# Optimization experiments

Hardware: AMD Instinct MI355X
Metric: run time of the kernel (lower is better)

Reference implementation:

```python
import jax, jax.numpy as jnp
import numpy as np

N, E, G = 50000, 800000, 64
DIMS = [(32, 4, 64), (256, 4, 128), (512, 4, 64)]
EPS = 1e-5  # BatchNorm eps (eval mode, running mean=0, var=1)


def setup_inputs():
    key = jax.random.key(0)
    ks = list(jax.random.split(key, 40))
    it = iter(range(40))
    nxt = lambda: ks[next(it)]
    inp = {}
    inp['x'] = jax.random.normal(nxt(), (N, 32), jnp.float32)
    inp['edge_feature'] = jax.random.normal(nxt(), (E, 6), jnp.float32)
    for li, (fin, H, C) in enumerate(DIMS, 1):
        s = 1.0 / np.sqrt(fin).astype(np.float32)
        inp[f'W{li}'] = jax.random.normal(nxt(), (fin, H * C), jnp.float32) * s
        inp[f'We{li}'] = jax.random.normal(nxt(), (6, H * C), jnp.float32) * 0.3
        inp[f'as{li}'] = jax.random.normal(nxt(), (H, C), jnp.float32) * 0.1
        inp[f'ad{li}'] = jax.random.normal(nxt(), (H, C), jnp.float32) * 0.1
        inp[f'ae{li}'] = jax.random.normal(nxt(), (H, C), jnp.float32) * 0.1
        inp[f'b{li}'] = jnp.zeros((H * C,), jnp.float32)
        inp[f'g{li}'] = jnp.ones((H * C,), jnp.float32)
        inp[f'bb{li}'] = jnp.zeros((H * C,), jnp.float32)
    inp['Wf1'] = jax.random.normal(nxt(), (256, 32), jnp.float32) * 0.0625
    inp['bf1'] = jnp.zeros((32,), jnp.float32)
    inp['gf'] = jnp.ones((32,), jnp.float32)
    inp['bbf'] = jnp.zeros((32,), jnp.float32)
    inp['Wf2'] = jax.random.normal(nxt(), (32, 2), jnp.float32) * 0.2
    inp['bf2'] = jnp.zeros((2,), jnp.float32)
    inp['edge_index'] = jax.random.randint(nxt(), (2, E), 0, N)
    inp['batch'] = jnp.sort(jax.random.randint(nxt(), (N,), 0, G))
    return inp


def _bn(h, g, b):
    # eval-mode BatchNorm1d with running mean 0, running var 1
    return g * h * (1.0 / jnp.sqrt(1.0 + EPS)) + b


def _gat(h, ea, src, dst, W, We, a_s, a_d, a_e, b):
    H, C = a_s.shape
    xs = (h @ W).reshape(N, H, C)                       # shared lin for src/dst
    al_s = jnp.einsum('nhc,hc->nh', xs, a_s)
    al_d = jnp.einsum('nhc,hc->nh', xs, a_d)
    al_e = jnp.einsum('ehc,hc->eh', (ea @ We).reshape(-1, H, C), a_e)
    al = jax.nn.leaky_relu(al_s[src] + al_d[dst] + al_e, 0.2)  # [E+N, H]
    m = jax.ops.segment_max(al, dst, num_segments=N)
    w = jnp.exp(al - m[dst])
    w = w / (jax.ops.segment_sum(w, dst, num_segments=N)[dst] + 1e-16)
    out = jax.ops.segment_sum(xs[src] * w[:, :, None], dst, num_segments=N)
    return out.reshape(N, H * C) + b


def _forward(x, edge_feature, W1, We1, as1, ad1, ae1, b1, g1, bb1,
             W2, We2, as2, ad2, ae2, b2, g2, bb2,
             W3, We3, as3, ad3, ae3, b3, g3, bb3,
             Wf1, bf1, gf, bbf, Wf2, bf2, edge_index, batch):
    src0, dst0 = edge_index[0], edge_index[1]
    # add self loops; self-loop edge_attr = per-dst mean (PyG fill_value='mean')
    deg = jax.ops.segment_sum(jnp.ones((E,), x.dtype), dst0, num_segments=N)
    emean = jax.ops.segment_sum(edge_feature, dst0, num_segments=N) / jnp.maximum(deg, 1.0)[:, None]
    loops = jnp.arange(N)
    src = jnp.concatenate([src0, loops])
    dst = jnp.concatenate([dst0, loops])
    ea = jnp.concatenate([edge_feature, emean], axis=0)
    h = jax.nn.elu(_bn(_gat(x, ea, src, dst, W1, We1, as1, ad1, ae1, b1), g1, bb1))
    h = jax.nn.elu(_bn(_gat(h, ea, src, dst, W2, We2, as2, ad2, ae2, b2), g2, bb2))
    h = jax.nn.elu(_bn(_gat(h, ea, src, dst, W3, We3, as3, ad3, ae3, b3), g3, bb3))
    cnt = jax.ops.segment_sum(jnp.ones((N,), h.dtype), batch, num_segments=G)
    pooled = jax.ops.segment_sum(h, batch, num_segments=G) / jnp.maximum(cnt, 1.0)[:, None]
    h = jax.nn.elu(_bn(pooled @ Wf1 + bf1, gf, bbf))
    return jax.nn.log_softmax(h @ Wf2 + bf2, axis=1)


def reference(x, edge_feature, W1, We1, as1, ad1, ae1, b1, g1, bb1,
              W2, We2, as2, ad2, ae2, b2, g2, bb2,
              W3, We3, as3, ad3, ae3, b3, g3, bb3,
              Wf1, bf1, gf, bbf, Wf2, bf2, edge_index, batch):
    return _forward(x, edge_feature, W1, We1, as1, ad1, ae1, b1, g1, bb1,
                    W2, We2, as2, ad2, ae2, b2, g2, bb2,
                    W3, We3, as3, ad3, ae3, b3, g3, bb3,
                    Wf1, bf1, gf, bbf, Wf2, bf2, edge_index, batch)
```

## Files before the change

### kernel.cpp

```cpp
#include <hip/hip_runtime.h>
#include <cstdint>
#include <cstddef>

#define NN 50000
#define NPAD 50048
#define EE 800000
#define ET (EE + NN)
#define GG 64
#define HH 4
#define RSQ 0.9999950000374997f

typedef short bf16x8 __attribute__((ext_vector_type(8)));
typedef unsigned short u16x8 __attribute__((ext_vector_type(8)));
typedef unsigned short u16x4 __attribute__((ext_vector_type(4)));
typedef float f32x4 __attribute__((ext_vector_type(4)));
typedef float f32x2 __attribute__((ext_vector_type(2)));

__device__ __forceinline__ float bf2f(unsigned short u) {
    union { unsigned int i; float f; } v; v.i = ((unsigned int)u) << 16; return v.f;
}
__device__ __forceinline__ unsigned short f2bf(float f) {
    union { float f; unsigned int i; } v; v.f = f;
    unsigned int u = v.i;
    u += 0x7fffu + ((u >> 16) & 1u);
    return (unsigned short)(u >> 16);
}


#if __has_builtin(__builtin_amdgcn_cvt_pk_fp8_f32) && __has_builtin(__builtin_amdgcn_cvt_pk_f32_fp8)
#define FP8_HW 1
#else
#define FP8_HW 0
#endif

#if !FP8_HW
__device__ __forceinline__ unsigned int enc1_fp8(float f) {
    unsigned int u = __float_as_uint(f);
    unsigned int s = (u >> 24) & 0x80u;
    float a = fabsf(f);
    a = fminf(a, 448.f);
    unsigned int b;
    if (a >= 0.015625f) {
        unsigned int ub = __float_as_uint(a);
        unsigned int mant = ub & 0x7FFFFFu;
        unsigned int keep = mant >> 20;
        unsigned int rem = mant & 0xFFFFFu;
        unsigned int exp = (ub >> 23) - 127u + 7u;
        unsigned int q = (exp << 3) | keep;
        if (rem > 0x80000u || (rem == 0x80000u && (q & 1u))) q++;
        if (q > 0x7Eu) q = 0x7Eu;
        b = q;
    } else {
        int q = (int)(a * 512.0f + 0.5f);
        b = (q > 7) ? 0x08u : (unsigned int)q;
    }
    return s | b;
}
__device__ __forceinline__ float dec1_fp8(unsigned int b) {
    unsigned int sgn = (b & 0x80u) << 24;
    float r;
    if (b & 0x78u) {
        r = __uint_as_float(sgn | (((b & 0x7Fu) + 0x3C0u) << 20));
    } else {
        r = (float)(b & 7u) * 0x1p-9f;
        r = (b & 0x80u) ? -r : r;
    }
    return r;
}
#endif

__device__ __forceinline__ unsigned int pk4_fp8(float f0, float f1, float f2, float f3) {
#if FP8_HW
    int r = __builtin_amdgcn_cvt_pk_fp8_f32(f0, f1, 0, false);
    r = __builtin_amdgcn_cvt_pk_fp8_f32(f2, f3, r, true);
    return (unsigned int)r;
#else
    return enc1_fp8(f0) | (enc1_fp8(f1) << 8) | (enc1_fp8(f2) << 16) | (enc1_fp8(f3) << 24);
#endif
}

__device__ __forceinline__ f32x2 dec2lo_fp8(unsigned int u) {
#if FP8_HW
    return __builtin_amdgcn_cvt_pk_f32_fp8((int)u, false);
#else
    f32x2 r; r[0] = dec1_fp8(u & 0xFFu); r[1] = dec1_fp8((u >> 8) & 0xFFu); return r;
#endif
}
__device__ __forceinline__ f32x2 dec2hi_fp8(unsigned int u) {
#if FP8_HW
    return __builtin_amdgcn_cvt_pk_f32_fp8((int)u, true);
#else
    f32x2 r; r[0] = dec1_fp8((u >> 16) & 0xFFu); r[1] = dec1_fp8(u >> 24); return r;
#endif
}

static inline void* carve(char*& p, size_t bytes) {
    void* r = (void*)p;
    p += (bytes + 255) & ~(size_t)255;
    return r;
}


__global__ void deg_kernel(const int* __restrict__ dst0, int* __restrict__ deg,
                           int* __restrict__ epos) {
    int e = blockIdx.x * blockDim.x + threadIdx.x;
    if (e >= EE) return;
    epos[e] = atomicAdd(&deg[dst0[e]], 1);
}

#define SCAN_B 512
__global__ void scan1_kernel(const int* __restrict__ deg, int* __restrict__ out,
                             int* __restrict__ bsum, int n) {
    __shared__ int tmp[SCAN_B];
    int i = blockIdx.x * SCAN_B + threadIdx.x;
    int v = (i < n) ? (deg[i] + 1) : 0;
    tmp[threadIdx.x] = v;
    __syncthreads();
    for (int off = 1; off < SCAN_B; off <<= 1) {
        int t = (threadIdx.x >= off) ? tmp[threadIdx.x - off] : 0;
        __syncthreads();
        tmp[threadIdx.x] += t;
        __syncthreads();
    }
    if (i < n) out[i] = tmp[threadIdx.x] - v;
    if (threadIdx.x == SCAN_B - 1) bsum[blockIdx.x] = tmp[threadIdx.x];
}

__global__ void scan2_kernel(int* __restrict__ bsum, int nb) {
    __shared__ int tmp[128];
    int v = (threadIdx.x < nb) ? bsum[threadIdx.x] : 0;
    tmp[threadIdx.x] = v;
    __syncthreads();
    for (int off = 1; off < 128; off <<= 1) {
        int t = (threadIdx.x >= off) ? tmp[threadIdx.x - off] : 0;
        __syncthreads();
        tmp[threadIdx.x] += t;
        __syncthreads();
    }
    if (threadIdx.x < nb) bsum[threadIdx.x] = tmp[threadIdx.x] - v;
}

__global__ void scan3_kernel(int* __restrict__ out, const int* __restrict__ bsum, int n) {
    int i = blockIdx.x * SCAN_B + threadIdx.x;
    if (i < n) out[i] += bsum[blockIdx.x];
    if (i == 0 && blockIdx.x == 0) out[n] = ET;
}

__global__ void fill_kernel(const int* __restrict__ src0, const int* __restrict__ dst0,
                            const int* __restrict__ row_ptr, const int* __restrict__ epos,
                            const int* __restrict__ deg,
                            int* __restrict__ ssrc, int* __restrict__ seid) {
    int e = blockIdx.x * blockDim.x + threadIdx.x;
    if (e < EE) {
        int idx = row_ptr[dst0[e]] + epos[e];
        ssrc[idx] = src0[e];
        seid[idx] = e;
    } else if (e < ET) {
        int n = e - EE;
        int idx = row_ptr[n] + deg[n];
        ssrc[idx] = n;
        seid[idx] = EE + n;
    }
}


__global__ void convx_kernel(const float* __restrict__ x, unsigned short* __restrict__ xb) {
    int i = blockIdx.x * blockDim.x + threadIdx.x;
    if (i >= NPAD * 64) return;
    int row = i >> 6, col = i & 63;
    float v = 0.f;
    if (row < NN && col < 32) v = x[(size_t)row * 32 + col];
    xb[i] = f2bf(v);
}

__global__ void convw_all_kernel(const float* __restrict__ W1, const float* __restrict__ W2,
                                 const float* __restrict__ W3,
                                 unsigned short* __restrict__ Wt1,
                                 unsigned short* __restrict__ Wt2,
                                 unsigned short* __restrict__ Wt3) {
    int i = blockIdx.x * blockDim.x + threadIdx.x;
    if (i < 16384) {
        int c = i >> 6, k = i & 63;
        Wt1[i] = (k < 32) ? f2bf(W1[(size_t)k * 256 + c]) : (unsigned short)0;
    } else if (i < 16384 + 131072) {
        int j = i - 16384;
        int c = j >> 8, k = j & 255;
        Wt2[j] = f2bf(W2[(size_t)k * 512 + c]);
    } else if (i < 16384 + 262144) {
        int j = i - 147456;
        int c = j >> 9, k = j & 511;
        Wt3[j] = f2bf(W3[(size_t)k * 256 + c]);
    }
}

__global__ void wea_all_kernel(const float* __restrict__ We1, const float* __restrict__ ae1,
                               const float* __restrict__ We2, const float* __restrict__ ae2,
                               const float* __restrict__ We3, const float* __restrict__ ae3,
                               float* __restrict__ Wea) {
    int t = threadIdx.x;
    if (t >= 72) return;
    int l = t / 24, w = t % 24, k = w / 4, h = w % 4;
    const float* We = (l == 0) ? We1 : (l == 1) ? We2 : We3;
    const float* ae = (l == 0) ? ae1 : (l == 1) ? ae2 : ae3;
    int C = (l == 1) ? 128 : 64;
    int HC = 4 * C;
    float s = 0.f;
    for (int c = 0; c < C; c++) s += We[(size_t)k * HC + h * C + c] * ae[(size_t)h * C + c];
    Wea[l * 24 + k * 4 + h] = s;
}


#if __has_builtin(__builtin_amdgcn_global_load_lds)
#define GLL_OK 1
#else
#define GLL_OK 0
#endif

#define TILE_LD 136

template <int C_>
__global__ __launch_bounds__(256) void gemm_fused_kernel(const unsigned short* __restrict__ A,
                                                         const unsigned short* __restrict__ Bt,
                                                         unsigned char* __restrict__ X8,
                                                         const float* __restrict__ a_s,
                                                         const float* __restrict__ a_d,
                                                         float* __restrict__ als,
                                                         float* __restrict__ ald,
                                                         int K) {
    constexpr int HC = HH * C_;
    __shared__ unsigned short smem[128 * TILE_LD + 64];
    unsigned short* As = smem;
    unsigned short* Bs = smem + 8192;
    const int tid = threadIdx.x;
    const int bm = blockIdx.x * 128;
    const int bn = blockIdx.y * 128;
    const int lane = tid & 63;
    const int wv = tid >> 6;
    const int wrow = (wv >> 1) * 64;
    const int wcol = (wv & 1) * 64;
    const int l15 = lane & 15;
    const int q = lane >> 4;

    f32x4 acc[4][4];
#pragma unroll
    for (int m = 0; m < 4; m++)
#pragma unroll
        for (int n = 0; n < 4; n++) acc[m][n] = (f32x4)0.f;

    for (int k0 = 0; k0 < K; k0 += 64) {
#pragma unroll
        for (int i = 0; i < 4; i++) {
            int c = (wv * 4 + i) * 64 + lane;
            int row = c >> 3, slot = c & 7;
            int slotG = slot ^ (row & 7);
            const unsigned short* ga = &A[(size_t)(bm + row) * K + k0 + slotG * 8];
            const unsigned short* gb = &Bt[(size_t)(bn + row) * K + k0 + slotG * 8];
#if GLL_OK
            __builtin_amdgcn_global_load_lds(
                (const __attribute__((address_space(1))) unsigned int*)ga,
                (__attribute__((address_space(3))) unsigned int*)&As[(size_t)(wv * 4 + i) * 512],
                16, 0, 0);
            __builtin_amdgcn_global_load_lds(
                (const __attribute__((address_space(1))) unsigned int*)gb,
                (__attribute__((address_space(3))) unsigned int*)&Bs[(size_t)(wv * 4 + i) * 512],
                16, 0, 0);
#else
            *(u16x8*)&As[(size_t)c * 8] = *(const u16x8*)ga;
            *(u16x8*)&Bs[(size_t)c * 8] = *(const u16x8*)gb;
#endif
        }
        __syncthreads();
#pragma unroll
        for (int kk = 0; kk < 2; kk++) {
            bf16x8 af[4], bfr[4];
#pragma unroll
            for (int m = 0; m < 4; m++) {
                int ra = wrow + m * 16 + l15;
                af[m] = *(const bf16x8*)&As[ra * 64 + ((kk * 4 + q) ^ (ra & 7)) * 8];
            }
#pragma unroll
            for (int n = 0; n < 4; n++) {
                int rb = wcol + n * 16 + l15;
                bfr[n] = *(const bf16x8*)&Bs[rb * 64 + ((kk * 4 + q) ^ (rb & 7)) * 8];
            }
#pragma unroll
            for (int m = 0; m < 4; m++)
#pragma unroll
                for (int n = 0; n < 4; n++)
                    acc[m][n] = __builtin_amdgcn_mfma_f32_16x16x32_bf16(af[m], bfr[n], acc[m][n], 0, 0, 0);
        }
        __syncthreads();
    }

    unsigned short* tile = smem;
#pragma unroll
    for (int m = 0; m < 4; m++) {
#pragma unroll
        for (int n = 0; n < 4; n++) {
#pragma unroll
            for (int j = 0; j < 4; j++) {
                int r = wrow + m * 16 + (lane >> 4) * 4 + j;
                int c = wcol + n * 16 + l15;
                tile[r * TILE_LD + c] = f2bf(acc[m][n][j]);
            }
        }
    }
    __syncthreads();

    const int tcol = tid & 15;
    const int trow = tid >> 4;
    float as8[8], ad8[8];
#pragma unroll
    for (int k = 0; k < 8; k++) {
        as8[k] = a_s[bn + tcol * 8 + k];
        ad8[k] = a_d[bn + tcol * 8 + k];
    }
#pragma unroll
    for (int i = 0; i < 8; i++) {
        int r = i * 16 + trow;
        int grow = bm + r;
        u16x8 v = *(const u16x8*)&tile[r * TILE_LD + tcol * 8];
        float f[8];
#pragma unroll
        for (int k = 0; k < 8; k++) f[k] = bf2f(v[k]);
        unsigned int r0 = pk4_fp8(f[0], f[1], f[2], f[3]);
        unsigned int r1 = pk4_fp8(f[4], f[5], f[6], f[7]);
        *(uint2*)&X8[(size_t)grow * HC + bn + tcol * 8] = make_uint2(r0, r1);
        float ps = 0.f, pd = 0.f;
#pragma unroll
        for (int k = 0; k < 8; k++) { ps += f[k] * as8[k]; pd += f[k] * ad8[k]; }
        if constexpr (C_ == 64) {
            ps += __shfl_xor(ps, 1); pd += __shfl_xor(pd, 1);
            ps += __shfl_xor(ps, 2); pd += __shfl_xor(pd, 2);
            ps += __shfl_xor(ps, 4); pd += __shfl_xor(pd, 4);
            if ((tid & 7) == 0 && grow < NN) {
                int head = (bn >> 6) + (tcol >> 3);
                als[(size_t)grow * HH + head] = ps;
                ald[(size_t)grow * HH + head] = pd;
            }
        } else {
            ps += __shfl_xor(ps, 1); pd += __shfl_xor(pd, 1);
            ps += __shfl_xor(ps, 2); pd += __shfl_xor(pd, 2);
            ps += __shfl_xor(ps, 4); pd += __shfl_xor(pd, 4);
            ps += __shfl_xor(ps, 8); pd += __shfl_xor(pd, 8);
            if ((tid & 15) == 0 && grow < NN) {
                int head = bn >> 7;
                als[(size_t)grow * HH + head] = ps;
                ald[(size_t)grow * HH + head] = pd;
            }
        }
    }
}


__global__ __launch_bounds__(256) void logits_softmax_kernel(
        const int* __restrict__ rowptr, const int* __restrict__ ssrc,
        const int* __restrict__ seid, const float* __restrict__ ef,
        const float* __restrict__ Wea,
        const float* __restrict__ als, const float* __restrict__ ald,
        float* __restrict__ al, float4* __restrict__ mM, float4* __restrict__ mR) {
    int wid = (blockIdx.x * blockDim.x + threadIdx.x) >> 6;
    int lane = threadIdx.x & 63;
    if (wid >= NN) return;
    int b = rowptr[wid], e = rowptr[wid + 1];
    int cnt = e - b;
    float4 ad4 = *(const float4*)&ald[(size_t)wid * 4];
    float inv = 1.0f / fmaxf((float)(cnt - 1), 1.0f);

    float m0 = -1e30f, m1 = -1e30f, m2 = -1e30f, m3 = -1e30f;
    float s0 = 0.f, s1 = 0.f, s2 = 0.f, s3 = 0.f;

    if (cnt <= 64) {
        bool has = (lane < cnt);
        int i = b + lane;
        int eid = has ? seid[i] : EE;
        int s = has ? ssrc[i] : 0;
        float ev[6] = {0.f, 0.f, 0.f, 0.f, 0.f, 0.f};
        bool real = has && (eid < EE);
        if (real) {
            const float* ep = &ef[(size_t)eid * 6];
#pragma unroll
            for (int k = 0; k < 6; k++) ev[k] = ep[k];
        }
        float es[6];
#pragma unroll
        for (int k = 0; k < 6; k++) es[k] = ev[k];
#pragma unroll
        for (int off = 32; off; off >>= 1)
#pragma unroll
            for (int k = 0; k < 6; k++) es[k] += __shfl_xor(es[k], off);
        if (has && eid >= EE) {
#pragma unroll
            for (int k = 0; k < 6; k++) ev[k] = es[k] * inv;
        }
        float4 as4 = make_float4(0.f, 0.f, 0.f, 0.f);
        if (has) as4 = *(const float4*)&als[(size_t)s * 4];
        float o[4] = {as4.x + ad4.x, as4.y + ad4.y, as4.z + ad4.z, as4.w + ad4.w};
#pragma unroll
        for (int h = 0; h < 4; h++) {
#pragma unroll
            for (int k = 0; k < 6; k++) o[h] += ev[k] * Wea[k * 4 + h];
            o[h] = o[h] > 0.f ? o[h] : 0.2f * o[h];
        }
        if (has) *(float4*)&al[(size_t)i * 4] = make_float4(o[0], o[1], o[2], o[3]);
        if (has) { m0 = o[0]; m1 = o[1]; m2 = o[2]; m3 = o[3]; }
#pragma unroll
        for (int off = 32; off; off >>= 1) {
            m0 = fmaxf(m0, __shfl_xor(m0, off)); m1 = fmaxf(m1, __shfl_xor(m1, off));
            m2 = fmaxf(m2, __shfl_xor(m2, off)); m3 = fmaxf(m3, __shfl_xor(m3, off));
        }
        if (has) {
            s0 = __expf(o[0] - m0); s1 = __expf(o[1] - m1);
            s2 = __expf(o[2] - m2); s3 = __expf(o[3] - m3);
        }
    } else {
        float es[6] = {0.f, 0.f, 0.f, 0.f, 0.f, 0.f};
        for (int i = b + lane; i < e; i += 64) {
            int eid = seid[i];
            if (eid < EE) {
                const float* ep = &ef[(size_t)eid * 6];
#pragma unroll
                for (int k = 0; k < 6; k++) es[k] += ep[k];
            }
        }
#pragma unroll
        for (int off = 32; off; off >>= 1)
#pragma unroll
            for (int k = 0; k < 6; k++) es[k] += __shfl_xor(es[k], off);
        float em[6];
#pragma unroll
        for (int k = 0; k < 6; k++) em[k] = es[k] * inv;

        for (int i = b + lane; i < e; i += 64) {
            int eid = seid[i];
            int s = ssrc[i];
            float4 as4 = *(const float4*)&als[(size_t)s * 4];
            float ev[6];
            if (eid < EE) {
                const float* ep = &ef[(size_t)eid * 6];
#pragma unroll
                for (int k = 0; k < 6; k++) ev[k] = ep[k];
            } else {
#pragma unroll
                for (int k = 0; k < 6; k++) ev[k] = em[k];
            }
            float o[4] = {as4.x + ad4.x, as4.y + ad4.y, as4.z + ad4.z, as4.w + ad4.w};
#pragma unroll
            for (int h = 0; h < 4; h++) {
#pragma unroll
                for (int k = 0; k < 6; k++) o[h] += ev[k] * Wea[k * 4 + h];
                o[h] = o[h] > 0.f ? o[h] : 0.2f * o[h];
            }
            *(float4*)&al[(size_t)i * 4] = make_float4(o[0], o[1], o[2], o[3]);
            m0 = fmaxf(m0, o[0]); m1 = fmaxf(m1, o[1]);
            m2 = fmaxf(m2, o[2]); m3 = fmaxf(m3, o[3]);
        }
#pragma unroll
        for (int off = 32; off; off >>= 1) {
            m0 = fmaxf(m0, __shfl_xor(m0, off)); m1 = fmaxf(m1, __shfl_xor(m1, off));
            m2 = fmaxf(m2, __shfl_xor(m2, off)); m3 = fmaxf(m3, __shfl_xor(m3, off));
        }
        for (int i = b + lane; i < e; i += 64) {
            float4 v = *(const float4*)&al[(size_t)i * 4];
            s0 += __expf(v.x - m0); s1 += __expf(v.y - m1);
            s2 += __expf(v.z - m2); s3 += __expf(v.w - m3);
        }
    }
#pragma unroll
    for (int off = 32; off; off >>= 1) {
        s0 += __shfl_xor(s0, off); s1 += __shfl_xor(s1, off);
        s2 += __shfl_xor(s2, off); s3 += __shfl_xor(s3, off);
    }
    if (lane == 0) {
        mM[wid] = make_float4(m0, m1, m2, m3);
        mR[wid] = make_float4(1.f / (s0 + 1e-16f), 1.f / (s1 + 1e-16f),
                              1.f / (s2 + 1e-16f), 1.f / (s3 + 1e-16f));
    }
}


template <int C_>
__global__ __launch_bounds__(256) void aggregate_kernel(const unsigned char* __restrict__ xs8,
                                                        const float* __restrict__ al,
                                                        const float4* __restrict__ mM,
                                                        const float4* __restrict__ mR,
                                                        const int* __restrict__ rowptr,
                                                        const int* __restrict__ ssrc,
                                                        const float* __restrict__ bias,
                                                        const float* __restrict__ gam,
                                                        const float* __restrict__ bet,
                                                        unsigned short* __restrict__ hout) {
    constexpr int HC = HH * C_;
    constexpr int BPL = HC / 32;
    int wid = (blockIdx.x * blockDim.x + threadIdx.x) >> 6;
    int lane = threadIdx.x & 63;
    if (wid >= NN) return;
    int b = rowptr[wid], e = rowptr[wid + 1];
    const int hpre = lane >> 4;
    const int m15 = lane & 15;
    const int lane32 = lane & 31;
    const int pairSel = lane >> 5;
    const int hself = lane32 >> 3;

    float4 mm4 = mM[wid];
    float4 rr4 = mR[wid];
    float mh = (hpre == 0) ? mm4.x : (hpre == 1) ? mm4.y : (hpre == 2) ? mm4.z : mm4.w;
    float rh = (hpre == 0) ? rr4.x : (hpre == 1) ? rr4.y : (hpre == 2) ? rr4.z : rr4.w;

    f32x2 acc2[BPL / 2];
#pragma unroll
    for (int k = 0; k < BPL / 2; k++) acc2[k] = (f32x2)0.f;

    const unsigned char* xbase = xs8 + (size_t)lane32 * BPL;

    for (int base = b; base < e; base += 64) {
        int cnt = e - base; if (cnt > 64) cnt = 64;
        int spre = (base + lane < e) ? ssrc[base + lane] : wid;
        float wpre[4];
#pragma unroll
        for (int q = 0; q < 4; q++) {
            int idx = base + q * 16 + m15;
            wpre[q] = (idx < e) ? __expf(al[(size_t)idx * 4 + hpre] - mh) * rh : 0.f;
        }
        int cnt8 = (cnt + 7) & ~7;
        for (int j = 0; j < cnt8; j += 8) {
            float ww[4];
            if constexpr (BPL == 16) {
                uint4 pk[4];
#pragma unroll
                for (int u = 0; u < 4; u++) {
                    int jj = j + 2 * u + pairSel;
                    int s = __shfl(spre, jj);
                    ww[u] = __shfl(wpre[jj >> 4], (hself << 4) | (jj & 15));
                    pk[u] = *(const uint4*)(xbase + (size_t)s * HC);
                }
#pragma unroll
                for (int u = 0; u < 4; u++) {
                    f32x2 wv; wv[0] = ww[u]; wv[1] = ww[u];
                    acc2[0] += wv * dec2lo_fp8(pk[u].x);
                    acc2[1] += wv * dec2hi_fp8(pk[u].x);
                    acc2[2] += wv * dec2lo_fp8(pk[u].y);
                    acc2[3] += wv * dec2hi_fp8(pk[u].y);
                    acc2[4] += wv * dec2lo_fp8(pk[u].z);
                    acc2[5] += wv * dec2hi_fp8(pk[u].z);
                    acc2[6] += wv * dec2lo_fp8(pk[u].w);
                    acc2[7] += wv * dec2hi_fp8(pk[u].w);
                }
            } else {
                uint2 pk[4];
#pragma unroll
                for (int u = 0; u < 4; u++) {
                    int jj = j + 2 * u + pairSel;
                    int s = __shfl(spre, jj);
                    ww[u] = __shfl(wpre[jj >> 4], (hself << 4) | (jj & 15));
                    pk[u] = *(const uint2*)(xbase + (size_t)s * HC);
                }
#pragma unroll
                for (int u = 0; u < 4; u++) {
                    f32x2 wv; wv[0] = ww[u]; wv[1] = ww[u];
                    acc2[0] += wv * dec2lo_fp8(pk[u].x);
                    acc2[1] += wv * dec2hi_fp8(pk[u].x);
                    acc2[2] += wv * dec2lo_fp8(pk[u].y);
                    acc2[3] += wv * dec2hi_fp8(pk[u].y);
                }
            }
        }
    }

#pragma unroll
    for (int k = 0; k < BPL / 2; k++) {
        acc2[k][0] += __shfl_xor(acc2[k][0], 32);
        acc2[k][1] += __shfl_xor(acc2[k][1], 32);
    }

    if (lane < 32) {
        float acc[BPL];
#pragma unroll
        for (int k = 0; k < BPL / 2; k++) { acc[2 * k] = acc2[k][0]; acc[2 * k + 1] = acc2[k][1]; }
        int base_c = lane32 * BPL;
        unsigned int opk[BPL / 2];
#pragma unroll
        for (int q = 0; q < BPL / 4; q++) {
            float4 bi = *(const float4*)&bias[base_c + q * 4];
            float4 ga = *(const float4*)&gam[base_c + q * 4];
            float4 be = *(const float4*)&bet[base_c + q * 4];
            float vv[4];
            vv[0] = ga.x * (acc[q * 4 + 0] + bi.x) * RSQ + be.x;
            vv[1] = ga.y * (acc[q * 4 + 1] + bi.y) * RSQ + be.y;
            vv[2] = ga.z * (acc[q * 4 + 2] + bi.z) * RSQ + be.z;
            vv[3] = ga.w * (acc[q * 4 + 3] + bi.w) * RSQ + be.w;
#pragma unroll
            for (int k = 0; k < 4; k++) vv[k] = vv[k] > 0.f ? vv[k] : (__expf(vv[k]) - 1.0f);
            opk[q * 2 + 0] = (unsigned int)f2bf(vv[0]) | ((unsigned int)f2bf(vv[1]) << 16);
            opk[q * 2 + 1] = (unsigned int)f2bf(vv[2]) | ((unsigned int)f2bf(vv[3]) << 16);
        }
        if constexpr (BPL == 8) {
            *(uint4*)&hout[(size_t)wid * HC + base_c] = make_uint4(opk[0], opk[1], opk[2], opk[3]);
        } else {
            *(uint4*)&hout[(size_t)wid * HC + base_c] = make_uint4(opk[0], opk[1], opk[2], opk[3]);
            *(uint4*)&hout[(size_t)wid * HC + base_c + 8] = make_uint4(opk[4], opk[5], opk[6], opk[7]);
        }
    }
}


__global__ void bounds_kernel(const int* __restrict__ batch, int* __restrict__ first,
                              int* __restrict__ last) {
    int n = blockIdx.x * blockDim.x + threadIdx.x;
    if (n >= NN) return;
    int b = batch[n];
    if (n == 0 || batch[n - 1] != b) first[b] = n;
    if (n == NN - 1 || batch[n + 1] != b) last[b] = n;
}

#define PCHUNK 64
__global__ __launch_bounds__(256) void pool_kernel(const unsigned short* __restrict__ h3,
                                                   const int* __restrict__ batch,
                                                   float* __restrict__ pooled) {
    int c = threadIdx.x;
    int n0 = blockIdx.x * PCHUNK;
    int nend = min(n0 + PCHUNK, NN);
    if (n0 >= NN) return;
    float local = 0.f;
    int curg = batch[n0];
    for (int n = n0; n < nend; n++) {
        int g = batch[n];
        if (g != curg) {
            atomicAdd(&pooled[(size_t)curg * 256 + c], local);
            local = 0.f;
            curg = g;
        }
        local += bf2f(h3[(size_t)n * 256 + c]);
    }
    atomicAdd(&pooled[(size_t)curg * 256 + c], local);
}

__global__ void final_kernel(const float* __restrict__ pooled,
                             const int* __restrict__ first, const int* __restrict__ last,
                             const float* __restrict__ Wf1, const float* __restrict__ bf1,
                             const float* __restrict__ gf, const float* __restrict__ bbf,
                             const float* __restrict__ Wf2, const float* __restrict__ bf2,
                             float* __restrict__ out) {
    int g = blockIdx.x;
    int j = threadIdx.x;
    __shared__ float hh[32];
    float c = fmaxf((float)(last[g] - first[g] + 1), 1.0f);
    float inv = 1.0f / c;
    float acc = bf1[j];
    for (int i = 0; i < 256; i++) acc += (pooled[(size_t)g * 256 + i] * inv) * Wf1[(size_t)i * 32 + j];
    float v = gf[j] * acc * RSQ + bbf[j];
    hh[j] = v > 0.f ? v : (__expf(v) - 1.0f);
    __syncthreads();
    if (j == 0) {
        float l0 = bf2[0], l1 = bf2[1];
        for (int i = 0; i < 32; i++) {
            l0 += hh[i] * Wf2[i * 2 + 0];
            l1 += hh[i] * Wf2[i * 2 + 1];
        }
        float mx = fmaxf(l0, l1);
        float lse = mx + logf(__expf(l0 - mx) + __expf(l1 - mx));
        out[g * 2 + 0] = l0 - lse;
        out[g * 2 + 1] = l1 - lse;
    }
}


extern "C" void kernel_launch(void* const* d_in, const int* in_sizes, int n_in,
                              void* d_out, int out_size, void* d_ws, size_t ws_size,
                              hipStream_t stream) {
    (void)in_sizes; (void)n_in; (void)out_size; (void)ws_size;

    const float* x  = (const float*)d_in[0];
    const float* ef = (const float*)d_in[1];
    const float* W_[3]  = {(const float*)d_in[2],  (const float*)d_in[10], (const float*)d_in[18]};
    const float* We_[3] = {(const float*)d_in[3],  (const float*)d_in[11], (const float*)d_in[19]};
    const float* As_[3] = {(const float*)d_in[4],  (const float*)d_in[12], (const float*)d_in[20]};
    const float* Ad_[3] = {(const float*)d_in[5],  (const float*)d_in[13], (const float*)d_in[21]};
    const float* Ae_[3] = {(const float*)d_in[6],  (const float*)d_in[14], (const float*)d_in[22]};
    const float* Bi_[3] = {(const float*)d_in[7],  (const float*)d_in[15], (const float*)d_in[23]};
    const float* Ga_[3] = {(const float*)d_in[8],  (const float*)d_in[16], (const float*)d_in[24]};
    const float* Be_[3] = {(const float*)d_in[9],  (const float*)d_in[17], (const float*)d_in[25]};
    const float* Wf1 = (const float*)d_in[26];
    const float* bf1 = (const float*)d_in[27];
    const float* gf  = (const float*)d_in[28];
    const float* bbf = (const float*)d_in[29];
    const float* Wf2 = (const float*)d_in[30];
    const float* bf2 = (const float*)d_in[31];
    const int* eidx  = (const int*)d_in[32];
    const int* src0  = eidx;
    const int* dst0  = eidx + EE;
    const int* batch = (const int*)d_in[33];
    float* out = (float*)d_out;

    char* p = (char*)d_ws;
    unsigned short* B0 = (unsigned short*)carve(p, (size_t)NPAD * 512 * 2);
    unsigned short* B2 = (unsigned short*)carve(p, (size_t)NPAD * 512 * 2);
    unsigned char*  X8 = (unsigned char*)carve(p, (size_t)NPAD * 512);
    unsigned short* Wt1 = (unsigned short*)carve(p, (size_t)256 * 64 * 2);
    unsigned short* Wt2 = (unsigned short*)carve(p, (size_t)512 * 256 * 2);
    unsigned short* Wt3 = (unsigned short*)carve(p, (size_t)256 * 512 * 2);
    float* al     = (float*)carve(p, (size_t)ET * 4 * 4);
    float* als    = (float*)carve(p, (size_t)NN * 4 * 4);
    float* ald    = (float*)carve(p, (size_t)NN * 4 * 4);
    float4* mM    = (float4*)carve(p, (size_t)NN * 16);
    float4* mR    = (float4*)carve(p, (size_t)NN * 16);
    float* wea    = (float*)carve(p, 3 * 24 * 4);
    float* pooled = (float*)carve(p, (size_t)GG * 256 * 4);
    int* first  = (int*)carve(p, (size_t)GG * 4);
    int* last   = (int*)carve(p, (size_t)GG * 4);
    int* deg    = (int*)carve(p, (size_t)NN * 4);
    int* rowptr = (int*)carve(p, (size_t)(NN + 1) * 4);
    int* epos   = (int*)carve(p, (size_t)EE * 4);
    int* ssrc   = (int*)carve(p, (size_t)ET * 4);
    int* seid   = (int*)carve(p, (size_t)ET * 4);
    int* bsum   = (int*)carve(p, 512);

    hipMemsetAsync(deg, 0, (size_t)NN * 4, stream);
    hipMemsetAsync(pooled, 0, (size_t)GG * 256 * 4, stream);
    hipMemsetAsync(first, 0x00, (size_t)GG * 4, stream);
    hipMemsetAsync(last, 0xFF, (size_t)GG * 4, stream);

    deg_kernel<<<(EE + 255) / 256, 256, 0, stream>>>(dst0, deg, epos);

    int nb = (NN + SCAN_B - 1) / SCAN_B;
    scan1_kernel<<<nb, SCAN_B, 0, stream>>>(deg, rowptr, bsum, NN);
    scan2_kernel<<<1, 128, 0, stream>>>(bsum, nb);
    scan3_kernel<<<nb, SCAN_B, 0, stream>>>(rowptr, bsum, NN);
    fill_kernel<<<(ET + 255) / 256, 256, 0, stream>>>(src0, dst0, rowptr, epos, deg, ssrc, seid);

    convx_kernel<<<(NPAD * 64 + 255) / 256, 256, 0, stream>>>(x, B0);
    convw_all_kernel<<<(278528 + 255) / 256, 256, 0, stream>>>(W_[0], W_[1], W_[2], Wt1, Wt2, Wt3);
    wea_all_kernel<<<1, 128, 0, stream>>>(We_[0], Ae_[0], We_[1], Ae_[1], We_[2], Ae_[2], wea);

    int wblocks = (NN * 64 + 255) / 256;
    const int fpad[3] = {64, 256, 512};
    const int HCs[3] = {256, 512, 256};
    const int Cs[3]  = {64, 128, 64};
    const unsigned short* Wts[3] = {Wt1, Wt2, Wt3};
    const unsigned short* inb[3]  = {B0, B2, B0};
    unsigned short* outb[3]       = {B2, B0, B2};

    for (int li = 0; li < 3; li++) {
        int Kp = fpad[li], HC = HCs[li];
        dim3 gg(NPAD / 128, HC / 128);
        if (Cs[li] == 64)
            gemm_fused_kernel<64><<<gg, 256, 0, stream>>>(inb[li], Wts[li], X8,
                                                          As_[li], Ad_[li], als, ald, Kp);
        else
            gemm_fused_kernel<128><<<gg, 256, 0, stream>>>(inb[li], Wts[li], X8,
                                                           As_[li], Ad_[li], als, ald, Kp);

        logits_softmax_kernel<<<wblocks, 256, 0, stream>>>(rowptr, ssrc, seid, ef,
                                                           wea + li * 24, als, ald, al, mM, mR);

        if (Cs[li] == 64)
            aggregate_kernel<64><<<wblocks, 256, 0, stream>>>(X8, al, mM, mR, rowptr, ssrc,
                                                              Bi_[li], Ga_[li], Be_[li], outb[li]);
        else
            aggregate_kernel<128><<<wblocks, 256, 0, stream>>>(X8, al, mM, mR, rowptr, ssrc,
                                                               Bi_[li], Ga_[li], Be_[li], outb[li]);
    }

    bounds_kernel<<<(NN + 255) / 256, 256, 0, stream>>>(batch, first, last);
    pool_kernel<<<(NN + PCHUNK - 1) / PCHUNK, 256, 0, stream>>>(B2, batch, pooled);
    final_kernel<<<GG, 32, 0, stream>>>(pooled, first, last, Wf1, bf1, gf, bbf, Wf2, bf2, out);
}
```

Measured before the change: 495.1 us.

## Fuse attention logits/softmax into aggregation kernel, keep weights in registers

Merges the per-node logits+softmax kernel with the aggregation kernel, so for nodes with up to 64 incoming edges the normalized attention weights stay in registers and are shuffled straight into the gather loop. This drops the al write/read round trip, the mM/mR buffers and one launch per layer. The gather layout also changes: all 64 lanes now cover the channel dimension of one edge at a time, instead of two half-waves each handling alternate edges, which removes the final cross-half reduction but makes each per-lane load narrower. High-degree nodes still take the old path that writes al and re-reads it.

```diff
diff --git a/kernel.cpp b/kernel.cpp
--- a/kernel.cpp
+++ b/kernel.cpp
@@ -12,7 +12,6 @@
 
 typedef short bf16x8 __attribute__((ext_vector_type(8)));
 typedef unsigned short u16x8 __attribute__((ext_vector_type(8)));
-typedef unsigned short u16x4 __attribute__((ext_vector_type(4)));
 typedef float f32x4 __attribute__((ext_vector_type(4)));
 typedef float f32x2 __attribute__((ext_vector_type(2)));
 
@@ -353,31 +352,80 @@
 }
 
 
-__global__ __launch_bounds__(256) void logits_softmax_kernel(
+template <int C_>
+__global__ __launch_bounds__(256) void aggregate_fused_kernel(
+        const unsigned char* __restrict__ xs8,
         const int* __restrict__ rowptr, const int* __restrict__ ssrc,
         const int* __restrict__ seid, const float* __restrict__ ef,
         const float* __restrict__ Wea,
         const float* __restrict__ als, const float* __restrict__ ald,
-        float* __restrict__ al, float4* __restrict__ mM, float4* __restrict__ mR) {
+        float* __restrict__ al,
+        const float* __restrict__ bias, const float* __restrict__ gam,
+        const float* __restrict__ bet, unsigned short* __restrict__ hout) {
+    constexpr int HC = HH * C_;
+    constexpr int CPL = HC / 64;
     int wid = (blockIdx.x * blockDim.x + threadIdx.x) >> 6;
     int lane = threadIdx.x & 63;
     if (wid >= NN) return;
     int b = rowptr[wid], e = rowptr[wid + 1];
     int cnt = e - b;
+    const int hpre = lane >> 4;
+    const int m15 = lane & 15;
+    float inv = 1.0f / fmaxf((float)(cnt - 1), 1.0f);
     float4 ad4 = *(const float4*)&ald[(size_t)wid * 4];
-    float inv = 1.0f / fmaxf((float)(cnt - 1), 1.0f);
-
-    float m0 = -1e30f, m1 = -1e30f, m2 = -1e30f, m3 = -1e30f;
-    float s0 = 0.f, s1 = 0.f, s2 = 0.f, s3 = 0.f;
+
+    f32x2 acc2[CPL / 2];
+#pragma unroll
+    for (int k = 0; k < CPL / 2; k++) acc2[k] = (f32x2)0.f;
+    const unsigned char* xbase = xs8 + (size_t)lane * CPL;
+
+    auto accum_window = [&](int spre, const float* wpre, int cnt8) {
+        for (int j = 0; j < cnt8; j += 8) {
+            if constexpr (CPL == 8) {
+                uint2 pk[8];
+                float ww[8];
+#pragma unroll
+                for (int u = 0; u < 8; u++) {
+                    int jj = j + u;
+                    int s = __shfl(spre, jj);
+                    ww[u] = __shfl(wpre[jj >> 4], (hpre << 4) | (jj & 15));
+                    pk[u] = *(const uint2*)(xbase + (size_t)s * HC);
+                }
+#pragma unroll
+                for (int u = 0; u < 8; u++) {
+                    f32x2 wv; wv[0] = ww[u]; wv[1] = ww[u];
+                    acc2[0] += wv * dec2lo_fp8(pk[u].x);
+                    acc2[1] += wv * dec2hi_fp8(pk[u].x);
+                    acc2[2] += wv * dec2lo_fp8(pk[u].y);
+                    acc2[3] += wv * dec2hi_fp8(pk[u].y);
+                }
+            } else {
+                unsigned int pk[8];
+                float ww[8];
+#pragma unroll
+                for (int u = 0; u < 8; u++) {
+                    int jj = j + u;
+                    int s = __shfl(spre, jj);
+                    ww[u] = __shfl(wpre[jj >> 4], (hpre << 4) | (jj & 15));
+                    pk[u] = *(const unsigned int*)(xbase + (size_t)s * HC);
+                }
+#pragma unroll
+                for (int u = 0; u < 8; u++) {
+                    f32x2 wv; wv[0] = ww[u]; wv[1] = ww[u];
+                    acc2[0] += wv * dec2lo_fp8(pk[u]);
+                    acc2[1] += wv * dec2hi_fp8(pk[u]);
+                }
+            }
+        }
+    };
 
     if (cnt <= 64) {
         bool has = (lane < cnt);
         int i = b + lane;
         int eid = has ? seid[i] : EE;
-        int s = has ? ssrc[i] : 0;
+        int s = has ? ssrc[i] : wid;
         float ev[6] = {0.f, 0.f, 0.f, 0.f, 0.f, 0.f};
-        bool real = has && (eid < EE);
-        if (real) {
+        if (has && eid < EE) {
             const float* ep = &ef[(size_t)eid * 6];
 #pragma unroll
             for (int k = 0; k < 6; k++) ev[k] = ep[k];
@@ -402,17 +450,35 @@
             for (int k = 0; k < 6; k++) o[h] += ev[k] * Wea[k * 4 + h];
             o[h] = o[h] > 0.f ? o[h] : 0.2f * o[h];
         }
-        if (has) *(float4*)&al[(size_t)i * 4] = make_float4(o[0], o[1], o[2], o[3]);
-        if (has) { m0 = o[0]; m1 = o[1]; m2 = o[2]; m3 = o[3]; }
+        float m0 = has ? o[0] : -1e30f, m1 = has ? o[1] : -1e30f;
+        float m2 = has ? o[2] : -1e30f, m3 = has ? o[3] : -1e30f;
 #pragma unroll
         for (int off = 32; off; off >>= 1) {
             m0 = fmaxf(m0, __shfl_xor(m0, off)); m1 = fmaxf(m1, __shfl_xor(m1, off));
             m2 = fmaxf(m2, __shfl_xor(m2, off)); m3 = fmaxf(m3, __shfl_xor(m3, off));
         }
-        if (has) {
-            s0 = __expf(o[0] - m0); s1 = __expf(o[1] - m1);
-            s2 = __expf(o[2] - m2); s3 = __expf(o[3] - m3);
-        }
+        float w4[4];
+        w4[0] = has ? __expf(o[0] - m0) : 0.f;
+        w4[1] = has ? __expf(o[1] - m1) : 0.f;
+        w4[2] = has ? __expf(o[2] - m2) : 0.f;
+        w4[3] = has ? __expf(o[3] - m3) : 0.f;
+        float s0 = w4[0], s1 = w4[1], s2 = w4[2], s3 = w4[3];
+#pragma unroll
+        for (int off = 32; off; off >>= 1) {
+            s0 += __shfl_xor(s0, off); s1 += __shfl_xor(s1, off);
+            s2 += __shfl_xor(s2, off); s3 += __shfl_xor(s3, off);
+        }
+        w4[0] *= 1.f / (s0 + 1e-16f); w4[1] *= 1.f / (s1 + 1e-16f);
+        w4[2] *= 1.f / (s2 + 1e-16f); w4[3] *= 1.f / (s3 + 1e-16f);
+        float wpre[4];
+#pragma unroll
+        for (int q = 0; q < 4; q++) {
+            int srcl = q * 16 + m15;
+            float t0 = __shfl(w4[0], srcl), t1 = __shfl(w4[1], srcl);
+            float t2 = __shfl(w4[2], srcl), t3 = __shfl(w4[3], srcl);
+            wpre[q] = (hpre == 0) ? t0 : (hpre == 1) ? t1 : (hpre == 2) ? t2 : t3;
+        }
+        accum_window(s, wpre, (cnt + 7) & ~7);
     } else {
         float es[6] = {0.f, 0.f, 0.f, 0.f, 0.f, 0.f};
         for (int i = b + lane; i < e; i += 64) {
@@ -431,6 +497,7 @@
 #pragma unroll
         for (int k = 0; k < 6; k++) em[k] = es[k] * inv;
 
+        float m0 = -1e30f, m1 = -1e30f, m2 = -1e30f, m3 = -1e30f;
         for (int i = b + lane; i < e; i += 64) {
             int eid = seid[i];
             int s = ssrc[i];
@@ -460,146 +527,59 @@
             m0 = fmaxf(m0, __shfl_xor(m0, off)); m1 = fmaxf(m1, __shfl_xor(m1, off));
             m2 = fmaxf(m2, __shfl_xor(m2, off)); m3 = fmaxf(m3, __shfl_xor(m3, off));
         }
+        float s0 = 0.f, s1 = 0.f, s2 = 0.f, s3 = 0.f;
         for (int i = b + lane; i < e; i += 64) {
             float4 v = *(const float4*)&al[(size_t)i * 4];
             s0 += __expf(v.x - m0); s1 += __expf(v.y - m1);
             s2 += __expf(v.z - m2); s3 += __expf(v.w - m3);
         }
-    }
-#pragma unroll
-    for (int off = 32; off; off >>= 1) {
-        s0 += __shfl_xor(s0, off); s1 += __shfl_xor(s1, off);
-        s2 += __shfl_xor(s2, off); s3 += __shfl_xor(s3, off);
-    }
-    if (lane == 0) {
-        mM[wid] = make_float4(m0, m1, m2, m3);
-        mR[wid] = make_float4(1.f / (s0 + 1e-16f), 1.f / (s1 + 1e-16f),
-                              1.f / (s2 + 1e-16f), 1.f / (s3 + 1e-16f));
-    }
-}
-
-
-template <int C_>
-__global__ __launch_bounds__(256) void aggregate_kernel(const unsigned char* __restrict__ xs8,
-                                                        const float* __restrict__ al,
-                                                        const float4* __restrict__ mM,
-                                                        const float4* __restrict__ mR,
-                                                        const int* __restrict__ rowptr,
-                                                        const int* __restrict__ ssrc,
-                                                        const float* __restrict__ bias,
-                                                        const float* __restrict__ gam,
-                                                        const float* __restrict__ bet,
-                                                        unsigned short* __restrict__ hout) {
-    constexpr int HC = HH * C_;
-    constexpr int BPL = HC / 32;
-    int wid = (blockIdx.x * blockDim.x + threadIdx.x) >> 6;
-    int lane = threadIdx.x & 63;
-    if (wid >= NN) return;
-    int b = rowptr[wid], e = rowptr[wid + 1];
-    const int hpre = lane >> 4;
-    const int m15 = lane & 15;
-    const int lane32 = lane & 31;
-    const int pairSel = lane >> 5;
-    const int hself = lane32 >> 3;
-
-    float4 mm4 = mM[wid];
-    float4 rr4 = mR[wid];
-    float mh = (hpre == 0) ? mm4.x : (hpre == 1) ? mm4.y : (hpre == 2) ? mm4.z : mm4.w;
-    float rh = (hpre == 0) ? rr4.x : (hpre == 1) ? rr4.y : (hpre == 2) ? rr4.z : rr4.w;
-
-    f32x2 acc2[BPL / 2];
-#pragma unroll
-    for (int k = 0; k < BPL / 2; k++) acc2[k] = (f32x2)0.f;
-
-    const unsigned char* xbase = xs8 + (size_t)lane32 * BPL;
-
-    for (int base = b; base < e; base += 64) {
-        int cnt = e - base; if (cnt > 64) cnt = 64;
-        int spre = (base + lane < e) ? ssrc[base + lane] : wid;
-        float wpre[4];
-#pragma unroll
-        for (int q = 0; q < 4; q++) {
-            int idx = base + q * 16 + m15;
-            wpre[q] = (idx < e) ? __expf(al[(size_t)idx * 4 + hpre] - mh) * rh : 0.f;
-        }
-        int cnt8 = (cnt + 7) & ~7;
-        for (int j = 0; j < cnt8; j += 8) {
-            float ww[4];
-            if constexpr (BPL == 16) {
-                uint4 pk[4];
-#pragma unroll
-                for (int u = 0; u < 4; u++) {
-                    int jj = j + 2 * u + pairSel;
-                    int s = __shfl(spre, jj);
-                    ww[u] = __shfl(wpre[jj >> 4], (hself << 4) | (jj & 15));
-                    pk[u] = *(const uint4*)(xbase + (size_t)s * HC);
-                }
-#pragma unroll
-                for (int u = 0; u < 4; u++) {
-                    f32x2 wv; wv[0] = ww[u]; wv[1] = ww[u];
-                    acc2[0] += wv * dec2lo_fp8(pk[u].x);
-                    acc2[1] += wv * dec2hi_fp8(pk[u].x);
-                    acc2[2] += wv * dec2lo_fp8(pk[u].y);
-                    acc2[3] += wv * dec2hi_fp8(pk[u].y);
-                    acc2[4] += wv * dec2lo_fp8(pk[u].z);
-                    acc2[5] += wv * dec2hi_fp8(pk[u].z);
-                    acc2[6] += wv * dec2lo_fp8(pk[u].w);
-                    acc2[7] += wv * dec2hi_fp8(pk[u].w);
-                }
-            } else {
-                uint2 pk[4];
-#pragma unroll
-                for (int u = 0; u < 4; u++) {
-                    int jj = j + 2 * u + pairSel;
-                    int s = __shfl(spre, jj);
-                    ww[u] = __shfl(wpre[jj >> 4], (hself << 4) | (jj & 15));
-                    pk[u] = *(const uint2*)(xbase + (size_t)s * HC);
-                }
-#pragma unroll
-                for (int u = 0; u < 4; u++) {
-                    f32x2 wv; wv[0] = ww[u]; wv[1] = ww[u];
-                    acc2[0] += wv * dec2lo_fp8(pk[u].x);
-                    acc2[1] += wv * dec2hi_fp8(pk[u].x);
-                    acc2[2] += wv * dec2lo_fp8(pk[u].y);
-                    acc2[3] += wv * dec2hi_fp8(pk[u].y);
-                }
-            }
-        }
-    }
-
-#pragma unroll
-    for (int k = 0; k < BPL / 2; k++) {
-        acc2[k][0] += __shfl_xor(acc2[k][0], 32);
-        acc2[k][1] += __shfl_xor(acc2[k][1], 32);
-    }
-
-    if (lane < 32) {
-        float acc[BPL];
-#pragma unroll
-        for (int k = 0; k < BPL / 2; k++) { acc[2 * k] = acc2[k][0]; acc[2 * k + 1] = acc2[k][1]; }
-        int base_c = lane32 * BPL;
-        unsigned int opk[BPL / 2];
-#pragma unroll
-        for (int q = 0; q < BPL / 4; q++) {
-            float4 bi = *(const float4*)&bias[base_c + q * 4];
-            float4 ga = *(const float4*)&gam[base_c + q * 4];
-            float4 be = *(const float4*)&bet[base_c + q * 4];
-            float vv[4];
-            vv[0] = ga.x * (acc[q * 4 + 0] + bi.x) * RSQ + be.x;
-            vv[1] = ga.y * (acc[q * 4 + 1] + bi.y) * RSQ + be.y;
-            vv[2] = ga.z * (acc[q * 4 + 2] + bi.z) * RSQ + be.z;
-            vv[3] = ga.w * (acc[q * 4 + 3] + bi.w) * RSQ + be.w;
-#pragma unroll
-            for (int k = 0; k < 4; k++) vv[k] = vv[k] > 0.f ? vv[k] : (__expf(vv[k]) - 1.0f);
-            opk[q * 2 + 0] = (unsigned int)f2bf(vv[0]) | ((unsigned int)f2bf(vv[1]) << 16);
-            opk[q * 2 + 1] = (unsigned int)f2bf(vv[2]) | ((unsigned int)f2bf(vv[3]) << 16);
-        }
-        if constexpr (BPL == 8) {
-            *(uint4*)&hout[(size_t)wid * HC + base_c] = make_uint4(opk[0], opk[1], opk[2], opk[3]);
-        } else {
-            *(uint4*)&hout[(size_t)wid * HC + base_c] = make_uint4(opk[0], opk[1], opk[2], opk[3]);
-            *(uint4*)&hout[(size_t)wid * HC + base_c + 8] = make_uint4(opk[4], opk[5], opk[6], opk[7]);
-        }
+#pragma unroll
+        for (int off = 32; off; off >>= 1) {
+            s0 += __shfl_xor(s0, off); s1 += __shfl_xor(s1, off);
+            s2 += __shfl_xor(s2, off); s3 += __shfl_xor(s3, off);
+        }
+        float r0 = 1.f / (s0 + 1e-16f), r1 = 1.f / (s1 + 1e-16f);
+        float r2 = 1.f / (s2 + 1e-16f), r3 = 1.f / (s3 + 1e-16f);
+        float mh = (hpre == 0) ? m0 : (hpre == 1) ? m1 : (hpre == 2) ? m2 : m3;
+        float rh = (hpre == 0) ? r0 : (hpre == 1) ? r1 : (hpre == 2) ? r2 : r3;
+
+        for (int base = b; base < e; base += 64) {
+            int c = e - base; if (c > 64) c = 64;
+            int spre = (base + lane < e) ? ssrc[base + lane] : wid;
+            float wpre[4];
+#pragma unroll
+            for (int q = 0; q < 4; q++) {
+                int idx = base + q * 16 + m15;
+                wpre[q] = (idx < e) ? __expf(al[(size_t)idx * 4 + hpre] - mh) * rh : 0.f;
+            }
+            accum_window(spre, wpre, (c + 7) & ~7);
+        }
+    }
+
+    float acc[CPL];
+#pragma unroll
+    for (int k = 0; k < CPL / 2; k++) { acc[2 * k] = acc2[k][0]; acc[2 * k + 1] = acc2[k][1]; }
+    int base_c = lane * CPL;
+    unsigned int opk[CPL / 2];
+#pragma unroll
+    for (int q = 0; q < CPL / 4; q++) {
+        float4 bi = *(const float4*)&bias[base_c + q * 4];
+        float4 ga = *(const float4*)&gam[base_c + q * 4];
+        float4 be = *(const float4*)&bet[base_c + q * 4];
+        float vv[4];
+        vv[0] = ga.x * (acc[q * 4 + 0] + bi.x) * RSQ + be.x;
+        vv[1] = ga.y * (acc[q * 4 + 1] + bi.y) * RSQ + be.y;
+        vv[2] = ga.z * (acc[q * 4 + 2] + bi.z) * RSQ + be.z;
+        vv[3] = ga.w * (acc[q * 4 + 3] + bi.w) * RSQ + be.w;
+#pragma unroll
+        for (int k = 0; k < 4; k++) vv[k] = vv[k] > 0.f ? vv[k] : (__expf(vv[k]) - 1.0f);
+        opk[q * 2 + 0] = (unsigned int)f2bf(vv[0]) | ((unsigned int)f2bf(vv[1]) << 16);
+        opk[q * 2 + 1] = (unsigned int)f2bf(vv[2]) | ((unsigned int)f2bf(vv[3]) << 16);
+    }
+    if constexpr (CPL == 4) {
+        *(uint2*)&hout[(size_t)wid * HC + base_c] = make_uint2(opk[0], opk[1]);
+    } else {
+        *(uint4*)&hout[(size_t)wid * HC + base_c] = make_uint4(opk[0], opk[1], opk[2], opk[3]);
     }
 }
 
@@ -702,8 +682,6 @@
     float* al     = (float*)carve(p, (size_t)ET * 4 * 4);
     float* als    = (float*)carve(p, (size_t)NN * 4 * 4);
     float* ald    = (float*)carve(p, (size_t)NN * 4 * 4);
-    float4* mM    = (float4*)carve(p, (size_t)NN * 16);
-    float4* mR    = (float4*)carve(p, (size_t)NN * 16);
     float* wea    = (float*)carve(p, 3 * 24 * 4);
     float* pooled = (float*)carve(p, (size_t)GG * 256 * 4);
     int* first  = (int*)carve(p, (size_t)GG * 4);
@@ -750,15 +728,14 @@
             gemm_fused_kernel<128><<<gg, 256, 0, stream>>>(inb[li], Wts[li], X8,
                                                            As_[li], Ad_[li], als, ald, Kp);
 
-        logits_softmax_kernel<<<wblocks, 256, 0, stream>>>(rowptr, ssrc, seid, ef,
-                                                           wea + li * 24, als, ald, al, mM, mR);
-
         if (Cs[li] == 64)
-            aggregate_kernel<64><<<wblocks, 256, 0, stream>>>(X8, al, mM, mR, rowptr, ssrc,
-                                                              Bi_[li], Ga_[li], Be_[li], outb[li]);
+            aggregate_fused_kernel<64><<<wblocks, 256, 0, stream>>>(
+                X8, rowptr, ssrc, seid, ef, wea + li * 24, als, ald, al,
+                Bi_[li], Ga_[li], Be_[li], outb[li]);
         else
-            aggregate_kernel<128><<<wblocks, 256, 0, stream>>>(X8, al, mM, mR, rowptr, ssrc,
-                                                               Bi_[li], Ga_[li], Be_[li], outb[li]);
+            aggregate_fused_kernel<128><<<wblocks, 256, 0, stream>>>(
+                X8, rowptr, ssrc, seid, ef, wea + li * 24, als, ald, al,
+                Bi_[li], Ga_[li], Be_[li], outb[li]);
     }
 
     bounds_kernel<<<(NN + 255) / 256, 256, 0, stream>>>(batch, first, last);
```

Result: faster. 451.9 us (-8.7%).
